# Performance work log

Measured on AMD Instinct MI355X. Metric: run time of the kernel, lower is better.

## Reference

```python
import jax, jax.numpy as jnp
import numpy as np

DEPTH = 24; D_MODEL = 192; D_INNER = 384; D_STATE = 16; DT_RANK = 12; D_CONV = 4
H = 32; W = 3200; P = 16; NP = (W // P) * (H // P)  # 400 patches
NCLS = 22; BATCH = 4; EPS = 1e-5


def _rmsnorm(x, w):
    return x * jax.lax.rsqrt(jnp.mean(x * x, axis=-1, keepdims=True) + EPS) * w


def _causal_dwconv(x, w, b):
    # x: (B, L, D), w: (D, K) depthwise, left-padded causal conv (mamba conv1d)
    D = x.shape[-1]; K = w.shape[-1]
    xp = jnp.pad(jnp.swapaxes(x, 1, 2), ((0, 0), (0, 0), (K - 1, 0)))
    y = jax.lax.conv_general_dilated(xp, w[:, None, :], (1,), 'VALID',
            dimension_numbers=('NCH', 'OIH', 'NCH'), feature_group_count=D)
    return jnp.swapaxes(y + b[None, :, None], 1, 2)


def _selective_scan(x, dt, Bm, Cm, A, Dsk):
    # x, dt: (B, L, d); Bm, Cm: (B, L, n); A: (d, n); Dsk: (d,)
    dA = jnp.exp(dt[..., None] * A)                  # (B, L, d, n)
    dBx = (dt * x)[..., None] * Bm[:, :, None, :]    # (B, L, d, n)
    h0 = jnp.zeros((x.shape[0], x.shape[2], A.shape[1]), x.dtype)

    def step(h, inp):
        a, bx, c = inp
        h = a * h + bx
        return h, jnp.einsum('bdn,bn->bd', h, c)

    _, ys = jax.lax.scan(step, h0,
        (jnp.swapaxes(dA, 0, 1), jnp.swapaxes(dBx, 0, 1), jnp.swapaxes(Cm, 0, 1)))
    return jnp.swapaxes(ys, 0, 1) + x * Dsk


def _mamba_dir(xz, cw_l, cb_l, xpw, dtw, dtb, A, Dsk):
    xx, z = jnp.split(xz, 2, axis=-1)
    xx = jax.nn.silu(_causal_dwconv(xx, cw_l, cb_l))
    dbl = xx @ xpw.T                                  # (B, L, dt_rank + 2n)
    dt = jax.nn.softplus(dbl[..., :DT_RANK] @ dtw.T + dtb)
    Bm = dbl[..., DT_RANK:DT_RANK + D_STATE]
    Cm = dbl[..., DT_RANK + D_STATE:]
    y = _selective_scan(xx, dt, Bm, Cm, A, Dsk)
    return y * jax.nn.silu(z)


def _forward(x, pe_w, pe_b, cls_token, pos_embed, norm_w, in_proj_w, cw, cb,
             xproj_w, dtproj_w, dtproj_b, A_log, A_b_log, Dp, outproj_w,
             norm_f_w, head_w, head_b):
    B = x.shape[0]
    # patch embed: conv2d stride=kernel=16 on (B,1,H,W)
    y = jax.lax.conv_general_dilated(x[:, None], pe_w, (P, P), 'VALID',
            dimension_numbers=('NCHW', 'OIHW', 'NCHW')) + pe_b[None, :, None, None]
    tok = jnp.transpose(y, (0, 2, 3, 1)).reshape(B, -1, D_MODEL)   # (B, NP, D)
    tok = jnp.concatenate([jnp.broadcast_to(cls_token, (B, 1, D_MODEL)), tok], axis=1)
    tok = tok + pos_embed

    def layer_step(carry, p):
        hidden, residual = carry
        nw, ipw, cw_l, cb_l, xpw, dtw, dtb, Al, Abl, Dsk, opw = p
        residual = residual + hidden          # fused add (residual_in_fp32: all fp32)
        h = _rmsnorm(residual, nw)
        xz = h @ ipw.T                         # (B, L, 2*d_inner)
        y_f = _mamba_dir(xz, cw_l, cb_l, xpw, dtw, dtb, -jnp.exp(Al), Dsk)
        y_b = _mamba_dir(xz[:, ::-1], cw_l, cb_l, xpw, dtw, dtb, -jnp.exp(Abl), Dsk)[:, ::-1]
        return ((y_f + y_b) @ opw.T, residual), None

    # NOTE: source sets residual = x AND hidden = x before the loop, so the
    (hidden, residual), _ = jax.lax.scan(
        layer_step, (tok, tok),
        (norm_w, in_proj_w, cw, cb, xproj_w, dtproj_w, dtproj_b, A_log, A_b_log, Dp, outproj_w))
    out = _rmsnorm(residual + hidden, norm_f_w)
    return out[:, 0] @ head_w.T + head_b          # (B, n_classes)


def setup_inputs() -> dict:
    key = jax.random.key(0)
    ks = jax.random.split(key, 12)

    def n(k, shape, scale):
        return jax.random.normal(k, shape, jnp.float32) * scale

    a_init = jnp.tile(jnp.log(jnp.arange(1, D_STATE + 1, dtype=jnp.float32))[None, None, :],
                      (DEPTH, D_INNER, 1))
    return {
        'x': n(ks[0], (BATCH, H, W), 1.0),
        'pe_w': n(ks[1], (D_MODEL, 1, P, P), 1.0 / P),
        'pe_b': jnp.zeros((D_MODEL,), jnp.float32),
        'cls_token': n(ks[2], (1, 1, D_MODEL), 0.02),
        'pos_embed': n(ks[3], (1, NP + 1, D_MODEL), 0.02),
        'norm_w': jnp.ones((DEPTH, D_MODEL), jnp.float32),
        'in_proj_w': n(ks[4], (DEPTH, 2 * D_INNER, D_MODEL), D_MODEL ** -0.5),
        'cw': n(ks[5], (DEPTH, D_INNER, D_CONV), D_CONV ** -0.5),
        'cb': jnp.zeros((DEPTH, D_INNER), jnp.float32),
        'xproj_w': n(ks[6], (DEPTH, DT_RANK + 2 * D_STATE, D_INNER), D_INNER ** -0.5),
        'dtproj_w': n(ks[7], (DEPTH, D_INNER, DT_RANK), DT_RANK ** -0.5),
        'dtproj_b': n(ks[8], (DEPTH, D_INNER), 0.1),
        'A_log': a_init,
        'A_b_log': a_init,
        'Dp': jnp.ones((DEPTH, D_INNER), jnp.float32),
        'outproj_w': n(ks[9], (DEPTH, D_MODEL, D_INNER), D_INNER ** -0.5 / np.sqrt(DEPTH)),
        'norm_f_w': jnp.ones((D_MODEL,), jnp.float32),
        'head_w': n(ks[10], (NCLS, D_MODEL), D_MODEL ** -0.5),
        'head_b': jnp.zeros((NCLS,), jnp.float32),
    }


def reference(x, pe_w, pe_b, cls_token, pos_embed, norm_w, in_proj_w, cw, cb,
              xproj_w, dtproj_w, dtproj_b, A_log, A_b_log, Dp, outproj_w,
              norm_f_w, head_w, head_b):
    return _forward(x, pe_w, pe_b, cls_token, pos_embed, norm_w, in_proj_w, cw, cb,
                    xproj_w, dtproj_w, dtproj_b, A_log, A_b_log, Dp, outproj_w,
                    norm_f_w, head_w, head_b)
```

## Files before the change

### kernel.cpp

```cpp
#include <hip/hip_runtime.h>
#include <hip/hip_bf16.h>

#define DEPTH 24
#define DM 192
#define DI 384
#define DS 16
#define DR 12
#define LSEQ 401
#define BATCH 4
#define NTOK (BATCH*LSEQ)
#define NCLS 22
#define NC 16
#define TCH 26

__device__ __forceinline__ float silu_f(float x) { return x / (1.f + __expf(-x)); }

__global__ void patch_embed_k(const float* __restrict__ x,
                              const float* __restrict__ pe_w,
                              const float* __restrict__ pe_b,
                              const float* __restrict__ cls,
                              const float* __restrict__ pos,
                              float* __restrict__ residual, float* __restrict__ hidden)
{
    __shared__ float xp[4][256];
    int g0 = blockIdx.x * 4;
    int c = threadIdx.x;
    #pragma unroll
    for (int j = 0; j < 4; j++) {
        int g = g0 + j;
        int b = g / LSEQ, t = g % LSEQ;
        if (t != 0) {
            int p = t - 1, pi = p / 200, pj = p % 200;
            for (int i = c; i < 256; i += 192) {
                int pp = i >> 4, qq = i & 15;
                xp[j][i] = x[((size_t)(b * 32 + pi * 16 + pp)) * 3200 + pj * 16 + qq];
            }
        }
    }
    __syncthreads();
    float acc[4] = {0.f, 0.f, 0.f, 0.f};
    for (int k = 0; k < 256; k++) {
        float w = pe_w[c * 256 + k];
        #pragma unroll
        for (int j = 0; j < 4; j++) acc[j] += xp[j][k] * w;
    }
    #pragma unroll
    for (int j = 0; j < 4; j++) {
        int g = g0 + j;
        int t = g % LSEQ;
        float v = (t == 0) ? cls[c] : (acc[j] + pe_b[c]);
        v += pos[t * DM + c];
        residual[(size_t)g * DM + c] = v;
        hidden[(size_t)g * DM + c] = v;
    }
}

__global__ __launch_bounds__(192) void prenorm_k(
    const float* __restrict__ resin, float* __restrict__ hidden,
    float* __restrict__ resout, float* __restrict__ hnorm,
    const float* __restrict__ nw, float* __restrict__ dbl)
{
    __shared__ float wsum[3][4];
    int c = threadIdx.x;
    int t0 = blockIdx.x * 4;
    int wave = c >> 6, lane = c & 63;
    float r[4], s[4];
    #pragma unroll
    for (int j = 0; j < 4; j++) {
        int idx = (t0 + j) * DM + c;
        r[j] = resin[idx] + hidden[idx];
        s[j] = r[j] * r[j];
    }
    #pragma unroll
    for (int off = 32; off > 0; off >>= 1) {
        #pragma unroll
        for (int j = 0; j < 4; j++) s[j] += __shfl_down(s[j], off);
    }
    if (lane == 0) {
        #pragma unroll
        for (int j = 0; j < 4; j++) wsum[wave][j] = s[j];
    }
    __syncthreads();
    float nwv = nw[c];
    #pragma unroll
    for (int j = 0; j < 4; j++) {
        float tot = wsum[0][j] + wsum[1][j] + wsum[2][j];
        float rms = rsqrtf(tot / (float)DM + 1e-5f);
        int idx = (t0 + j) * DM + c;
        resout[idx] = r[j];
        hnorm[idx] = r[j] * rms * nwv;
        hidden[idx] = 0.f;
    }
    for (int i = blockIdx.x * 192 + c; i < 2 * NTOK * 44; i += 401 * 192)
        dbl[i] = 0.f;
}

__global__ __launch_bounds__(256) void gemm_xz_k(
    const float* __restrict__ hnorm, const float* __restrict__ ipw,
    float* __restrict__ xz)
{
    constexpr int KS = 48;
    __shared__ float As[KS][68];
    __shared__ float Ws[KS][68];
    int tid = threadIdx.x;
    int bn = blockIdx.x * 64;
    int bm = blockIdx.y * 64;
    int r0 = (tid >> 4) * 4;
    int c0 = (tid & 15) * 4;
    int srow = tid >> 2, sk = (tid & 3) * 12;
    float acc[4][4] = {};
    for (int k0 = 0; k0 < DM; k0 += KS) {
        {
            int m = bm + srow;
            const float* ap = hnorm + (size_t)m * DM + k0 + sk;
            #pragma unroll
            for (int i = 0; i < 12; i++)
                As[sk + i][srow] = (m < NTOK) ? ap[i] : 0.f;
            const float* wp = ipw + (size_t)(bn + srow) * DM + k0 + sk;
            #pragma unroll
            for (int i = 0; i < 12; i++)
                Ws[sk + i][srow] = wp[i];
        }
        __syncthreads();
        #pragma unroll
        for (int kk = 0; kk < KS; kk++) {
            float4 a = *(const float4*)&As[kk][r0];
            float4 w = *(const float4*)&Ws[kk][c0];
            acc[0][0] += a.x * w.x; acc[0][1] += a.x * w.y; acc[0][2] += a.x * w.z; acc[0][3] += a.x * w.w;
            acc[1][0] += a.y * w.x; acc[1][1] += a.y * w.y; acc[1][2] += a.y * w.z; acc[1][3] += a.y * w.w;
            acc[2][0] += a.z * w.x; acc[2][1] += a.z * w.y; acc[2][2] += a.z * w.z; acc[2][3] += a.z * w.w;
            acc[3][0] += a.w * w.x; acc[3][1] += a.w * w.y; acc[3][2] += a.w * w.z; acc[3][3] += a.w * w.w;
        }
        __syncthreads();
    }
    #pragma unroll
    for (int i = 0; i < 4; i++) {
        int m = bm + r0 + i;
        if (m >= NTOK) continue;
        *(float4*)&xz[(size_t)m * (2 * DI) + bn + c0] =
            make_float4(acc[i][0], acc[i][1], acc[i][2], acc[i][3]);
    }
}

__global__ __launch_bounds__(256) void xproj_conv_k(
    const float* __restrict__ xz,
    const float* __restrict__ cw, const float* __restrict__ cb,
    const float* __restrict__ xpw, float* __restrict__ dbl)
{
    __shared__ float As[96][33];
    __shared__ float Ws[96][48];
    int tid = threadIdx.x;
    int kbase = blockIdx.x * 96;
    int bm = blockIdx.y * 32;
    for (int idx = tid; idx < 96 * 32; idx += 256) {
        int k = idx >> 5, row = idx & 31;
        int m = bm + row;
        float v = 0.f;
        if (m < 2 * NTOK) {
            int dir = m / NTOK;
            int r = m - dir * NTOK;
            int b = r / LSEQ, t = r % LSEQ;
            int ch = kbase + k;
            float a = cb[ch];
            #pragma unroll
            for (int j = 0; j < 4; j++) {
                int tt = t - 3 + j;
                if (tt >= 0) {
                    int st = dir ? (LSEQ - 1 - tt) : tt;
                    a += cw[ch * 4 + j] * xz[((size_t)(b * LSEQ + st)) * (2 * DI) + ch];
                }
            }
            v = silu_f(a);
        }
        As[k][row] = v;
    }
    for (int i = tid; i < 96 * 48; i += 256) {
        int k = i / 48, rr = i % 48;
        Ws[k][rr] = (rr < 44) ? xpw[(size_t)rr * DI + kbase + k] : 0.f;
    }
    __syncthreads();
    int row = tid & 31, cg = tid >> 5;
    int cbase = cg * 6;
    float acc[6] = {};
    #pragma unroll 4
    for (int kk = 0; kk < 96; kk++) {
        float a = As[kk][row];
        #pragma unroll
        for (int j = 0; j < 6; j++) acc[j] += a * Ws[kk][cbase + j];
    }
    int m = bm + row;
    if (m < 2 * NTOK) {
        #pragma unroll
        for (int j = 0; j < 6; j++) {
            int cc = cbase + j;
            if (cc < 44) atomicAdd(&dbl[(size_t)m * 44 + cc], acc[j]);
        }
    }
}

__global__ __launch_bounds__(256) void scan_part_k(
    const float* __restrict__ xz, const float* __restrict__ dbl,
    const float* __restrict__ cw, const float* __restrict__ cb,
    const float* __restrict__ dtw, const float* __restrict__ dtb,
    const float* __restrict__ A_log, const float* __restrict__ A_b_log,
    float* __restrict__ hloc, float* __restrict__ Pc)
{
    __shared__ float sdbl[TCH][44];
    __shared__ float sdt[TCH][16];
    __shared__ float sxx[TCH][16];
    __shared__ float sw[16][12];
    __shared__ float sb2[16];
    int dblk = blockIdx.x, chunk = blockIdx.y;
    int db = blockIdx.z;
    int dir = db >> 2, b = db & 3;
    int tid = threadIdx.x;
    int d0 = dblk * 16;
    int t0 = chunk * TCH;
    size_t dof44 = (size_t)db * LSEQ * 44;
    for (int i = tid; i < TCH * 44; i += 256) {
        int t = i / 44, cc = i - t * 44;
        sdbl[t][cc] = dbl[dof44 + (size_t)(t0 + t) * 44 + cc];
    }
    if (tid < 192) { int d = tid / 12, r = tid - d * 12; sw[d][r] = dtw[(size_t)(d0 + d) * 12 + r]; }
    if (tid < 16) sb2[tid] = dtb[d0 + tid];
    for (int i = tid; i < TCH * 16; i += 256) {
        int t = i >> 4, d = i & 15;
        int tq = t0 + t, ch = d0 + d;
        float a = cb[ch];
        #pragma unroll
        for (int j = 0; j < 4; j++) {
            int tt = tq - 3 + j;
            if (tt >= 0) {
                int st = dir ? (LSEQ - 1 - tt) : tt;
                a += cw[ch * 4 + j] * xz[((size_t)(b * LSEQ + st)) * (2 * DI) + ch];
            }
        }
        sxx[t][d] = silu_f(a);
    }
    __syncthreads();
    for (int i = tid; i < TCH * 16; i += 256) {
        int t = i >> 4, d = i & 15;
        float a2 = sb2[d];
        #pragma unroll
        for (int r = 0; r < 12; r++) a2 += sdbl[t][r] * sw[d][r];
        sdt[t][d] = (a2 > 15.f) ? a2 : __logf(1.f + __expf(a2));
    }
    __syncthreads();
    int wave = tid >> 6, lane = tid & 63;
    int dsub = wave * 4 + (lane >> 4);
    int n = lane & 15;
    const float* Al = dir ? A_b_log : A_log;
    float Aval = -__expf(Al[(d0 + dsub) * DS + n]);
    float h = 0.f, P = 1.f;
    #pragma unroll
    for (int i = 0; i < TCH; i++) {
        float dtv = sdt[i][dsub];
        float xv  = sxx[i][dsub];
        float Bv  = sdbl[i][12 + n];
        float dA = __expf(dtv * Aval);
        h = dA * h + (dtv * xv) * Bv;
        P *= dA;
    }
    size_t idx2 = ((size_t)db * NC + chunk) * (DI * DS) + (size_t)(d0 + dsub) * DS + n;
    hloc[idx2] = h;
    Pc[idx2] = P;
}

__global__ __launch_bounds__(256) void scan_fix_k(
    const float* __restrict__ xz, const float* __restrict__ dbl,
    const float* __restrict__ cw, const float* __restrict__ cb,
    const float* __restrict__ dtw, const float* __restrict__ dtb,
    const float* __restrict__ A_log, const float* __restrict__ A_b_log,
    const float* __restrict__ Dp,
    const float* __restrict__ hloc, const float* __restrict__ Pc,
    float* __restrict__ yraw)
{
    __shared__ float sdbl[TCH][44];
    __shared__ float sdt[TCH][16];
    __shared__ float sxx[TCH][16];
    __shared__ float sy[TCH][16];
    __shared__ float sw[16][12];
    __shared__ float sb2[16];
    int dblk = blockIdx.x, chunk = blockIdx.y;
    int db = blockIdx.z;
    int dir = db >> 2, b = db & 3;
    int tid = threadIdx.x;
    int d0 = dblk * 16;
    int t0 = chunk * TCH;
    size_t dofD = (size_t)db * LSEQ * DI;
    size_t dof44 = (size_t)db * LSEQ * 44;
    for (int i = tid; i < TCH * 44; i += 256) {
        int t = i / 44, cc = i - t * 44;
        sdbl[t][cc] = ((t0 + t) < LSEQ) ? dbl[dof44 + (size_t)(t0 + t) * 44 + cc] : 0.f;
    }
    if (tid < 192) { int d = tid / 12, r = tid - d * 12; sw[d][r] = dtw[(size_t)(d0 + d) * 12 + r]; }
    if (tid < 16) sb2[tid] = dtb[d0 + tid];
    for (int i = tid; i < TCH * 16; i += 256) {
        int t = i >> 4, d = i & 15;
        int tq = t0 + t, ch = d0 + d;
        float v = 0.f;
        if (tq < LSEQ) {
            float a = cb[ch];
            #pragma unroll
            for (int j = 0; j < 4; j++) {
                int tt = tq - 3 + j;
                if (tt >= 0) {
                    int st = dir ? (LSEQ - 1 - tt) : tt;
                    a += cw[ch * 4 + j] * xz[((size_t)(b * LSEQ + st)) * (2 * DI) + ch];
                }
            }
            v = silu_f(a);
        }
        sxx[t][d] = v;
    }
    __syncthreads();
    for (int i = tid; i < TCH * 16; i += 256) {
        int t = i >> 4, d = i & 15;
        float a2 = sb2[d];
        #pragma unroll
        for (int r = 0; r < 12; r++) a2 += sdbl[t][r] * sw[d][r];
        sdt[t][d] = (a2 > 15.f) ? a2 : __logf(1.f + __expf(a2));
    }
    __syncthreads();
    int wave = tid >> 6, lane = tid & 63;
    int dsub = wave * 4 + (lane >> 4);
    int n = lane & 15;
    const float* Al = dir ? A_b_log : A_log;
    float Aval = -__expf(Al[(d0 + dsub) * DS + n]);
    float Dv = Dp[d0 + dsub];
    float h = 0.f;
    size_t cbase = (size_t)db * NC * (DI * DS) + (size_t)(d0 + dsub) * DS + n;
    #pragma unroll
    for (int j = 0; j < NC - 1; j++) {
        size_t idx = cbase + (size_t)j * (DI * DS);
        float pj = Pc[idx], hj = hloc[idx];
        h = (j < chunk) ? (pj * h + hj) : h;
    }
    #pragma unroll
    for (int i = 0; i < TCH; i++) {
        float dtv = sdt[i][dsub];
        float xv  = sxx[i][dsub];
        float Bv  = sdbl[i][12 + n];
        float Cv  = sdbl[i][28 + n];
        h = __expf(dtv * Aval) * h + (dtv * xv) * Bv;
        float p = h * Cv;
        p += __shfl_xor(p, 1);
        p += __shfl_xor(p, 2);
        p += __shfl_xor(p, 4);
        p += __shfl_xor(p, 8);
        if (n == 0) sy[i][dsub] = p + xv * Dv;
    }
    __syncthreads();
    int len = min(t0 + TCH, LSEQ) - t0;
    for (int idx = tid; idx < len * 16; idx += 256) {
        int t = idx >> 4, d = idx & 15;
        yraw[dofD + (size_t)(t0 + t) * DI + d0 + d] = sy[t][d];
    }
}

__global__ __launch_bounds__(256) void outproj_k(
    const float* __restrict__ yraw, const float* __restrict__ xz,
    const float* __restrict__ opw, float* __restrict__ hidden)
{
    __shared__ float As[96][34];
    __shared__ float Ws[96][34];
    int tid = threadIdx.x;
    int bn = blockIdx.x * 32;
    int bm = blockIdx.y * 32;
    int kbase = blockIdx.z * 192;
    int row8 = tid >> 3, seg = tid & 7, k0 = seg * 24;
    float a[24], wreg[24];
    int m = bm + row8;
    if (m < NTOK) {
        int b = m / LSEQ, t = m % LSEQ;
        const float* yf = yraw + (size_t)m * DI + kbase + k0;
        const float* yb = yraw + (size_t)(NTOK + b * LSEQ + (LSEQ - 1 - t)) * DI + kbase + k0;
        const float* zp = xz + (size_t)m * (2 * DI) + DI + kbase + k0;
        #pragma unroll
        for (int i = 0; i < 24; i++) {
            float z = zp[i];
            a[i] = (yf[i] + yb[i]) * (z / (1.f + __expf(-z)));
        }
    } else {
        #pragma unroll
        for (int i = 0; i < 24; i++) a[i] = 0.f;
    }
    {
        const float* wp = opw + (size_t)(bn + row8) * DI + kbase + k0;
        #pragma unroll
        for (int i = 0; i < 24; i++) wreg[i] = wp[i];
    }
    int r0 = (tid >> 4) * 2, c0 = (tid & 15) * 2;
    float acc[2][2] = {};
    #pragma unroll
    for (int st = 0; st < 2; st++) {
        if (st) __syncthreads();
        if ((seg >> 2) == st) {
            int kb = k0 - st * 96;
            #pragma unroll
            for (int i = 0; i < 24; i++) {
                As[kb + i][row8] = a[i];
                Ws[kb + i][row8] = wreg[i];
            }
        }
        __syncthreads();
        #pragma unroll 8
        for (int kk = 0; kk < 96; kk++) {
            float2 av = *(const float2*)&As[kk][r0];
            float2 wv = *(const float2*)&Ws[kk][c0];
            acc[0][0] += av.x * wv.x; acc[0][1] += av.x * wv.y;
            acc[1][0] += av.y * wv.x; acc[1][1] += av.y * wv.y;
        }
    }
    #pragma unroll
    for (int i = 0; i < 2; i++) {
        int mm = bm + r0 + i;
        if (mm >= NTOK) continue;
        #pragma unroll
        for (int j = 0; j < 2; j++)
            atomicAdd(&hidden[(size_t)mm * DM + bn + c0 + j], acc[i][j]);
    }
}

__global__ void final_head_k(const float* __restrict__ residual, const float* __restrict__ hidden,
                             const float* __restrict__ norm_f,
                             const float* __restrict__ head_w,
                             const float* __restrict__ head_b,
                             void* __restrict__ out,
                             const unsigned short* __restrict__ probe)
{
    __shared__ float wsum[3];
    __shared__ float hb[DM];
    int b = blockIdx.x;
    int c = threadIdx.x;
    int idx = (b * LSEQ) * DM + c;
    float r = residual[idx] + hidden[idx];
    float s = r * r;
    for (int off = 32; off > 0; off >>= 1) s += __shfl_down(s, off);
    int wave = c >> 6, lane = c & 63;
    if (lane == 0) wsum[wave] = s;
    __syncthreads();
    float tot = wsum[0] + wsum[1] + wsum[2];
    float rms = rsqrtf(tot / (float)DM + 1e-5f);
    hb[c] = r * rms * norm_f[c];
    __syncthreads();
    if (c < NCLS) {
        float acc = head_b[c];
        #pragma unroll 8
        for (int k = 0; k < DM; k++) acc += hb[k] * head_w[c * DM + k];
        if (probe[0] == 0x3F80u)
            ((__hip_bfloat16*)out)[b * NCLS + c] = __float2bfloat16(acc);
        else
            ((float*)out)[b * NCLS + c] = acc;
    }
}

extern "C" void kernel_launch(void* const* d_in, const int* in_sizes, int n_in,
                              void* d_out, int out_size, void* d_ws, size_t ws_size,
                              hipStream_t stream)
{
    (void)in_sizes; (void)n_in; (void)out_size; (void)ws_size;
    const float* x      = (const float*)d_in[0];
    const float* pe_w   = (const float*)d_in[1];
    const float* pe_b   = (const float*)d_in[2];
    const float* cls    = (const float*)d_in[3];
    const float* pos    = (const float*)d_in[4];
    const float* norm_w = (const float*)d_in[5];
    const float* ipw    = (const float*)d_in[6];
    const float* cw     = (const float*)d_in[7];
    const float* cb     = (const float*)d_in[8];
    const float* xpw    = (const float*)d_in[9];
    const float* dtw    = (const float*)d_in[10];
    const float* dtb    = (const float*)d_in[11];
    const float* A_log  = (const float*)d_in[12];
    const float* A_b_log= (const float*)d_in[13];
    const float* Dp     = (const float*)d_in[14];
    const float* opw    = (const float*)d_in[15];
    const float* norm_f = (const float*)d_in[16];
    const float* head_w = (const float*)d_in[17];
    const float* head_b = (const float*)d_in[18];
    const unsigned short* probe = (const unsigned short*)d_in[14];

    float* ws = (float*)d_ws;
    const size_t nTokDM = (size_t)NTOK * DM;
    const size_t nTokXZ = (size_t)NTOK * 2 * DI;
    const size_t nDirDI = (size_t)2 * NTOK * DI;
    const size_t nDir44 = (size_t)2 * NTOK * 44;
    const size_t nChunk = (size_t)2 * BATCH * NC * DI * DS;
    float* resA   = ws;
    float* resB   = resA + nTokDM;
    float* hidden = resB + nTokDM;
    float* hnorm  = hidden + nTokDM;
    float* xz     = hnorm + nTokDM;
    float* dbl    = xz + nTokXZ;
    float* yraw   = dbl + nDir44;
    float* hloc   = yraw + nDirDI;
    float* Pc     = hloc + nChunk;

    patch_embed_k<<<NTOK / 4, DM, 0, stream>>>(x, pe_w, pe_b, cls, pos, resA, hidden);

    for (int l = 0; l < DEPTH; l++) {
        float* rin  = (l & 1) ? resB : resA;
        float* rout = (l & 1) ? resA : resB;

        prenorm_k<<<LSEQ, DM, 0, stream>>>(rin, hidden, rout, hnorm,
                                           norm_w + (size_t)l * DM, dbl);

        gemm_xz_k<<<dim3(12, 26), 256, 0, stream>>>(
            hnorm, ipw + (size_t)l * 2 * DI * DM, xz);

        xproj_conv_k<<<dim3(4, 101), 256, 0, stream>>>(
            xz, cw + (size_t)l * DI * 4, cb + (size_t)l * DI,
            xpw + (size_t)l * 44 * DI, dbl);

        scan_part_k<<<dim3(DI / 16, NC - 1, 2 * BATCH), 256, 0, stream>>>(
            xz, dbl, cw + (size_t)l * DI * 4, cb + (size_t)l * DI,
            dtw + (size_t)l * DI * DR, dtb + (size_t)l * DI,
            A_log + (size_t)l * DI * DS, A_b_log + (size_t)l * DI * DS,
            hloc, Pc);

        scan_fix_k<<<dim3(DI / 16, NC, 2 * BATCH), 256, 0, stream>>>(
            xz, dbl, cw + (size_t)l * DI * 4, cb + (size_t)l * DI,
            dtw + (size_t)l * DI * DR, dtb + (size_t)l * DI,
            A_log + (size_t)l * DI * DS, A_b_log + (size_t)l * DI * DS,
            Dp + (size_t)l * DI, hloc, Pc, yraw);

        outproj_k<<<dim3(6, 51, 2), 256, 0, stream>>>(
            yraw, xz, opw + (size_t)l * DM * DI, hidden);
    }

    final_head_k<<<BATCH, DM, 0, stream>>>(resA, hidden, norm_f, head_w, head_b,
                                           d_out, probe);
}
```

Before: 3.061 ms.

## Fuse RMSNorm into in-proj GEMM, drop split-K atomics, use single-pass sequential scan

The standalone prenorm kernel is folded into the in-projection GEMM. Each block computes the residual sum and RMS for its rows, and the first column block writes the residual out. The x-projection and out-projection kernels loop over the full K dimension inside one block instead of splitting K across blocks, so they store results directly and no longer need atomics or buffer zeroing. The two-pass chunked scan (partial states plus fix-up) becomes one kernel per (channel block, direction×batch) that walks the sequence serially in 64-step tiles. This removes the hloc/Pc traffic and two launches per layer, but leaves far fewer blocks and a long serial dependency chain.

```diff
diff --git a/kernel.cpp b/kernel.cpp
--- a/kernel.cpp
+++ b/kernel.cpp
@@ -10,8 +10,7 @@
 #define BATCH 4
 #define NTOK (BATCH*LSEQ)
 #define NCLS 22
-#define NC 16
-#define TCH 26
+#define SCH 64
 
 __device__ __forceinline__ float silu_f(float x) { return x / (1.f + __expf(-x)); }
 
@@ -55,77 +54,80 @@
     }
 }
 
-__global__ __launch_bounds__(192) void prenorm_k(
-    const float* __restrict__ resin, float* __restrict__ hidden,
-    float* __restrict__ resout, float* __restrict__ hnorm,
-    const float* __restrict__ nw, float* __restrict__ dbl)
-{
-    __shared__ float wsum[3][4];
-    int c = threadIdx.x;
-    int t0 = blockIdx.x * 4;
-    int wave = c >> 6, lane = c & 63;
-    float r[4], s[4];
-    #pragma unroll
-    for (int j = 0; j < 4; j++) {
-        int idx = (t0 + j) * DM + c;
-        r[j] = resin[idx] + hidden[idx];
-        s[j] = r[j] * r[j];
-    }
-    #pragma unroll
-    for (int off = 32; off > 0; off >>= 1) {
-        #pragma unroll
-        for (int j = 0; j < 4; j++) s[j] += __shfl_down(s[j], off);
-    }
-    if (lane == 0) {
-        #pragma unroll
-        for (int j = 0; j < 4; j++) wsum[wave][j] = s[j];
-    }
-    __syncthreads();
-    float nwv = nw[c];
-    #pragma unroll
-    for (int j = 0; j < 4; j++) {
-        float tot = wsum[0][j] + wsum[1][j] + wsum[2][j];
-        float rms = rsqrtf(tot / (float)DM + 1e-5f);
-        int idx = (t0 + j) * DM + c;
-        resout[idx] = r[j];
-        hnorm[idx] = r[j] * rms * nwv;
-        hidden[idx] = 0.f;
-    }
-    for (int i = blockIdx.x * 192 + c; i < 2 * NTOK * 44; i += 401 * 192)
-        dbl[i] = 0.f;
-}
-
 __global__ __launch_bounds__(256) void gemm_xz_k(
-    const float* __restrict__ hnorm, const float* __restrict__ ipw,
-    float* __restrict__ xz)
-{
-    constexpr int KS = 48;
-    __shared__ float As[KS][68];
-    __shared__ float Ws[KS][68];
+    const float* __restrict__ resin, const float* __restrict__ hidden,
+    float* __restrict__ resout, const float* __restrict__ nw,
+    const float* __restrict__ ipw, float* __restrict__ xz)
+{
+    __shared__ float As[48][68];
+    __shared__ float Ws[48][68];
+    __shared__ float srms[64];
+    __shared__ float ps[64][4];
     int tid = threadIdx.x;
     int bn = blockIdx.x * 64;
     int bm = blockIdx.y * 64;
-    int r0 = (tid >> 4) * 4;
-    int c0 = (tid & 15) * 4;
-    int srow = tid >> 2, sk = (tid & 3) * 12;
+    int rr = tid >> 2, q = tid & 3;
+    int m = bm + rr;
+    float rv[4][12];
+    float s = 0.f;
+    if (m < NTOK) {
+        const float* rp = resin + (size_t)m * DM;
+        const float* hp = hidden + (size_t)m * DM;
+        #pragma unroll
+        for (int c = 0; c < 4; c++) {
+            int base = c * 48 + q * 12;
+            #pragma unroll
+            for (int i = 0; i < 12; i += 4) {
+                float4 a = *(const float4*)&rp[base + i];
+                float4 b = *(const float4*)&hp[base + i];
+                float r0 = a.x + b.x, r1 = a.y + b.y, r2 = a.z + b.z, r3 = a.w + b.w;
+                rv[c][i] = r0; rv[c][i + 1] = r1; rv[c][i + 2] = r2; rv[c][i + 3] = r3;
+                s += r0 * r0 + r1 * r1 + r2 * r2 + r3 * r3;
+            }
+        }
+        if (bn == 0) {
+            float* op = resout + (size_t)m * DM;
+            #pragma unroll
+            for (int c = 0; c < 4; c++) {
+                int base = c * 48 + q * 12;
+                #pragma unroll
+                for (int i = 0; i < 12; i += 4)
+                    *(float4*)&op[base + i] =
+                        make_float4(rv[c][i], rv[c][i + 1], rv[c][i + 2], rv[c][i + 3]);
+            }
+        }
+    } else {
+        #pragma unroll
+        for (int c = 0; c < 4; c++)
+            #pragma unroll
+            for (int i = 0; i < 12; i++) rv[c][i] = 0.f;
+    }
+    ps[rr][q] = s;
+    __syncthreads();
+    if (q == 0) {
+        float tot = ps[rr][0] + ps[rr][1] + ps[rr][2] + ps[rr][3];
+        srms[rr] = rsqrtf(tot * (1.f / (float)DM) + 1e-5f);
+    }
+    __syncthreads();
+
+    int orow = (tid >> 4) * 4;
+    int ocol = (tid & 15) * 4;
+    int sk = q * 12;
     float acc[4][4] = {};
-    for (int k0 = 0; k0 < DM; k0 += KS) {
-        {
-            int m = bm + srow;
-            const float* ap = hnorm + (size_t)m * DM + k0 + sk;
-            #pragma unroll
-            for (int i = 0; i < 12; i++)
-                As[sk + i][srow] = (m < NTOK) ? ap[i] : 0.f;
-            const float* wp = ipw + (size_t)(bn + srow) * DM + k0 + sk;
-            #pragma unroll
-            for (int i = 0; i < 12; i++)
-                Ws[sk + i][srow] = wp[i];
-        }
-        __syncthreads();
-        #pragma unroll
-        for (int kk = 0; kk < KS; kk++) {
-            float4 a = *(const float4*)&As[kk][r0];
-            float4 w = *(const float4*)&Ws[kk][c0];
+    for (int c = 0; c < 4; c++) {
+        float rs = srms[rr];
+        #pragma unroll
+        for (int i = 0; i < 12; i++)
+            As[sk + i][rr] = rv[c][i] * rs * nw[c * 48 + sk + i];
+        const float* wp = ipw + (size_t)(bn + rr) * DM + c * 48 + sk;
+        #pragma unroll
+        for (int i = 0; i < 12; i++)
+            Ws[sk + i][rr] = wp[i];
+        __syncthreads();
+        #pragma unroll
+        for (int kk = 0; kk < 48; kk++) {
+            float4 a = *(const float4*)&As[kk][orow];
+            float4 w = *(const float4*)&Ws[kk][ocol];
             acc[0][0] += a.x * w.x; acc[0][1] += a.x * w.y; acc[0][2] += a.x * w.z; acc[0][3] += a.x * w.w;
             acc[1][0] += a.y * w.x; acc[1][1] += a.y * w.y; acc[1][2] += a.y * w.z; acc[1][3] += a.y * w.w;
             acc[2][0] += a.z * w.x; acc[2][1] += a.z * w.y; acc[2][2] += a.z * w.z; acc[2][3] += a.z * w.w;
@@ -135,14 +137,14 @@
     }
     #pragma unroll
     for (int i = 0; i < 4; i++) {
-        int m = bm + r0 + i;
-        if (m >= NTOK) continue;
-        *(float4*)&xz[(size_t)m * (2 * DI) + bn + c0] =
+        int mm = bm + orow + i;
+        if (mm >= NTOK) continue;
+        *(float4*)&xz[(size_t)mm * (2 * DI) + bn + ocol] =
             make_float4(acc[i][0], acc[i][1], acc[i][2], acc[i][3]);
     }
 }
 
-__global__ __launch_bounds__(256) void xproj_conv_k(
+__global__ __launch_bounds__(256) void xproj_k(
     const float* __restrict__ xz,
     const float* __restrict__ cw, const float* __restrict__ cb,
     const float* __restrict__ xpw, float* __restrict__ dbl)
@@ -150,178 +152,78 @@
     __shared__ float As[96][33];
     __shared__ float Ws[96][48];
     int tid = threadIdx.x;
-    int kbase = blockIdx.x * 96;
-    int bm = blockIdx.y * 32;
-    for (int idx = tid; idx < 96 * 32; idx += 256) {
-        int k = idx >> 5, row = idx & 31;
-        int m = bm + row;
-        float v = 0.f;
-        if (m < 2 * NTOK) {
-            int dir = m / NTOK;
-            int r = m - dir * NTOK;
-            int b = r / LSEQ, t = r % LSEQ;
-            int ch = kbase + k;
-            float a = cb[ch];
-            #pragma unroll
-            for (int j = 0; j < 4; j++) {
-                int tt = t - 3 + j;
-                if (tt >= 0) {
-                    int st = dir ? (LSEQ - 1 - tt) : tt;
-                    a += cw[ch * 4 + j] * xz[((size_t)(b * LSEQ + st)) * (2 * DI) + ch];
-                }
-            }
-            v = silu_f(a);
-        }
-        As[k][row] = v;
-    }
-    for (int i = tid; i < 96 * 48; i += 256) {
-        int k = i / 48, rr = i % 48;
-        Ws[k][rr] = (rr < 44) ? xpw[(size_t)rr * DI + kbase + k] : 0.f;
-    }
-    __syncthreads();
+    int bm = blockIdx.x * 32;
     int row = tid & 31, cg = tid >> 5;
     int cbase = cg * 6;
     float acc[6] = {};
-    #pragma unroll 4
-    for (int kk = 0; kk < 96; kk++) {
-        float a = As[kk][row];
-        #pragma unroll
-        for (int j = 0; j < 6; j++) acc[j] += a * Ws[kk][cbase + j];
-    }
-    int m = bm + row;
-    if (m < 2 * NTOK) {
+    for (int kbase = 0; kbase < DI; kbase += 96) {
+        for (int idx = tid; idx < 96 * 32; idx += 256) {
+            int k = idx >> 5, r = idx & 31;
+            int mm = bm + r;
+            float v = 0.f;
+            if (mm < 2 * NTOK) {
+                int dir = mm / NTOK;
+                int rem = mm - dir * NTOK;
+                int b = rem / LSEQ, t = rem % LSEQ;
+                int ch = kbase + k;
+                float a = cb[ch];
+                #pragma unroll
+                for (int j = 0; j < 4; j++) {
+                    int tt = t - 3 + j;
+                    if (tt >= 0) {
+                        int st = dir ? (LSEQ - 1 - tt) : tt;
+                        a += cw[ch * 4 + j] * xz[((size_t)(b * LSEQ + st)) * (2 * DI) + ch];
+                    }
+                }
+                v = silu_f(a);
+            }
+            As[k][r] = v;
+        }
+        for (int i = tid; i < 96 * 48; i += 256) {
+            int k = i / 48, cc = i % 48;
+            Ws[k][cc] = (cc < 44) ? xpw[(size_t)cc * DI + kbase + k] : 0.f;
+        }
+        __syncthreads();
+        #pragma unroll 4
+        for (int kk = 0; kk < 96; kk++) {
+            float a = As[kk][row];
+            #pragma unroll
+            for (int j = 0; j < 6; j++) acc[j] += a * Ws[kk][cbase + j];
+        }
+        __syncthreads();
+    }
+    int mm = bm + row;
+    if (mm < 2 * NTOK) {
         #pragma unroll
         for (int j = 0; j < 6; j++) {
             int cc = cbase + j;
-            if (cc < 44) atomicAdd(&dbl[(size_t)m * 44 + cc], acc[j]);
-        }
-    }
-}
-
-__global__ __launch_bounds__(256) void scan_part_k(
+            if (cc < 44) dbl[(size_t)mm * 44 + cc] = acc[j];
+        }
+    }
+}
+
+__global__ __launch_bounds__(256) void scan_k(
     const float* __restrict__ xz, const float* __restrict__ dbl,
     const float* __restrict__ cw, const float* __restrict__ cb,
     const float* __restrict__ dtw, const float* __restrict__ dtb,
     const float* __restrict__ A_log, const float* __restrict__ A_b_log,
-    float* __restrict__ hloc, float* __restrict__ Pc)
-{
-    __shared__ float sdbl[TCH][44];
-    __shared__ float sdt[TCH][16];
-    __shared__ float sxx[TCH][16];
+    const float* __restrict__ Dp, float* __restrict__ yraw)
+{
+    __shared__ float sdbl[SCH][44];
+    __shared__ float sxx[SCH][16];
+    __shared__ float sdt[SCH][16];
+    __shared__ float sy[SCH][16];
     __shared__ float sw[16][12];
     __shared__ float sb2[16];
-    int dblk = blockIdx.x, chunk = blockIdx.y;
-    int db = blockIdx.z;
+    int dblk = blockIdx.x;
+    int db = blockIdx.y;
     int dir = db >> 2, b = db & 3;
     int tid = threadIdx.x;
     int d0 = dblk * 16;
-    int t0 = chunk * TCH;
     size_t dof44 = (size_t)db * LSEQ * 44;
-    for (int i = tid; i < TCH * 44; i += 256) {
-        int t = i / 44, cc = i - t * 44;
-        sdbl[t][cc] = dbl[dof44 + (size_t)(t0 + t) * 44 + cc];
-    }
+    size_t dofD = (size_t)db * LSEQ * DI;
     if (tid < 192) { int d = tid / 12, r = tid - d * 12; sw[d][r] = dtw[(size_t)(d0 + d) * 12 + r]; }
     if (tid < 16) sb2[tid] = dtb[d0 + tid];
-    for (int i = tid; i < TCH * 16; i += 256) {
-        int t = i >> 4, d = i & 15;
-        int tq = t0 + t, ch = d0 + d;
-        float a = cb[ch];
-        #pragma unroll
-        for (int j = 0; j < 4; j++) {
-            int tt = tq - 3 + j;
-            if (tt >= 0) {
-                int st = dir ? (LSEQ - 1 - tt) : tt;
-                a += cw[ch * 4 + j] * xz[((size_t)(b * LSEQ + st)) * (2 * DI) + ch];
-            }
-        }
-        sxx[t][d] = silu_f(a);
-    }
-    __syncthreads();
-    for (int i = tid; i < TCH * 16; i += 256) {
-        int t = i >> 4, d = i & 15;
-        float a2 = sb2[d];
-        #pragma unroll
-        for (int r = 0; r < 12; r++) a2 += sdbl[t][r] * sw[d][r];
-        sdt[t][d] = (a2 > 15.f) ? a2 : __logf(1.f + __expf(a2));
-    }
-    __syncthreads();
-    int wave = tid >> 6, lane = tid & 63;
-    int dsub = wave * 4 + (lane >> 4);
-    int n = lane & 15;
-    const float* Al = dir ? A_b_log : A_log;
-    float Aval = -__expf(Al[(d0 + dsub) * DS + n]);
-    float h = 0.f, P = 1.f;
-    #pragma unroll
-    for (int i = 0; i < TCH; i++) {
-        float dtv = sdt[i][dsub];
-        float xv  = sxx[i][dsub];
-        float Bv  = sdbl[i][12 + n];
-        float dA = __expf(dtv * Aval);
-        h = dA * h + (dtv * xv) * Bv;
-        P *= dA;
-    }
-    size_t idx2 = ((size_t)db * NC + chunk) * (DI * DS) + (size_t)(d0 + dsub) * DS + n;
-    hloc[idx2] = h;
-    Pc[idx2] = P;
-}
-
-__global__ __launch_bounds__(256) void scan_fix_k(
-    const float* __restrict__ xz, const float* __restrict__ dbl,
-    const float* __restrict__ cw, const float* __restrict__ cb,
-    const float* __restrict__ dtw, const float* __restrict__ dtb,
-    const float* __restrict__ A_log, const float* __restrict__ A_b_log,
-    const float* __restrict__ Dp,
-    const float* __restrict__ hloc, const float* __restrict__ Pc,
-    float* __restrict__ yraw)
-{
-    __shared__ float sdbl[TCH][44];
-    __shared__ float sdt[TCH][16];
-    __shared__ float sxx[TCH][16];
-    __shared__ float sy[TCH][16];
-    __shared__ float sw[16][12];
-    __shared__ float sb2[16];
-    int dblk = blockIdx.x, chunk = blockIdx.y;
-    int db = blockIdx.z;
-    int dir = db >> 2, b = db & 3;
-    int tid = threadIdx.x;
-    int d0 = dblk * 16;
-    int t0 = chunk * TCH;
-    size_t dofD = (size_t)db * LSEQ * DI;
-    size_t dof44 = (size_t)db * LSEQ * 44;
-    for (int i = tid; i < TCH * 44; i += 256) {
-        int t = i / 44, cc = i - t * 44;
-        sdbl[t][cc] = ((t0 + t) < LSEQ) ? dbl[dof44 + (size_t)(t0 + t) * 44 + cc] : 0.f;
-    }
-    if (tid < 192) { int d = tid / 12, r = tid - d * 12; sw[d][r] = dtw[(size_t)(d0 + d) * 12 + r]; }
-    if (tid < 16) sb2[tid] = dtb[d0 + tid];
-    for (int i = tid; i < TCH * 16; i += 256) {
-        int t = i >> 4, d = i & 15;
-        int tq = t0 + t, ch = d0 + d;
-        float v = 0.f;
-        if (tq < LSEQ) {
-            float a = cb[ch];
-            #pragma unroll
-            for (int j = 0; j < 4; j++) {
-                int tt = tq - 3 + j;
-                if (tt >= 0) {
-                    int st = dir ? (LSEQ - 1 - tt) : tt;
-                    a += cw[ch * 4 + j] * xz[((size_t)(b * LSEQ + st)) * (2 * DI) + ch];
-                }
-            }
-            v = silu_f(a);
-        }
-        sxx[t][d] = v;
-    }
-    __syncthreads();
-    for (int i = tid; i < TCH * 16; i += 256) {
-        int t = i >> 4, d = i & 15;
-        float a2 = sb2[d];
-        #pragma unroll
-        for (int r = 0; r < 12; r++) a2 += sdbl[t][r] * sw[d][r];
-        sdt[t][d] = (a2 > 15.f) ? a2 : __logf(1.f + __expf(a2));
-    }
-    __syncthreads();
     int wave = tid >> 6, lane = tid & 63;
     int dsub = wave * 4 + (lane >> 4);
     int n = lane & 15;
@@ -329,32 +231,55 @@
     float Aval = -__expf(Al[(d0 + dsub) * DS + n]);
     float Dv = Dp[d0 + dsub];
     float h = 0.f;
-    size_t cbase = (size_t)db * NC * (DI * DS) + (size_t)(d0 + dsub) * DS + n;
-    #pragma unroll
-    for (int j = 0; j < NC - 1; j++) {
-        size_t idx = cbase + (size_t)j * (DI * DS);
-        float pj = Pc[idx], hj = hloc[idx];
-        h = (j < chunk) ? (pj * h + hj) : h;
-    }
-    #pragma unroll
-    for (int i = 0; i < TCH; i++) {
-        float dtv = sdt[i][dsub];
-        float xv  = sxx[i][dsub];
-        float Bv  = sdbl[i][12 + n];
-        float Cv  = sdbl[i][28 + n];
-        h = __expf(dtv * Aval) * h + (dtv * xv) * Bv;
-        float p = h * Cv;
-        p += __shfl_xor(p, 1);
-        p += __shfl_xor(p, 2);
-        p += __shfl_xor(p, 4);
-        p += __shfl_xor(p, 8);
-        if (n == 0) sy[i][dsub] = p + xv * Dv;
-    }
-    __syncthreads();
-    int len = min(t0 + TCH, LSEQ) - t0;
-    for (int idx = tid; idx < len * 16; idx += 256) {
-        int t = idx >> 4, d = idx & 15;
-        yraw[dofD + (size_t)(t0 + t) * DI + d0 + d] = sy[t][d];
+    for (int t0 = 0; t0 < LSEQ; t0 += SCH) {
+        int len = min(LSEQ - t0, SCH);
+        for (int i = tid; i < len * 44; i += 256) {
+            int t = i / 44, cc = i - t * 44;
+            sdbl[t][cc] = dbl[dof44 + (size_t)(t0 + t) * 44 + cc];
+        }
+        for (int i = tid; i < len * 16; i += 256) {
+            int t = i >> 4, d = i & 15;
+            int tq = t0 + t, ch = d0 + d;
+            float a = cb[ch];
+            #pragma unroll
+            for (int j = 0; j < 4; j++) {
+                int tt = tq - 3 + j;
+                if (tt >= 0) {
+                    int st = dir ? (LSEQ - 1 - tt) : tt;
+                    a += cw[ch * 4 + j] * xz[((size_t)(b * LSEQ + st)) * (2 * DI) + ch];
+                }
+            }
+            sxx[t][d] = silu_f(a);
+        }
+        __syncthreads();
+        for (int i = tid; i < len * 16; i += 256) {
+            int t = i >> 4, d = i & 15;
+            float a2 = sb2[d];
+            #pragma unroll
+            for (int r = 0; r < 12; r++) a2 += sdbl[t][r] * sw[d][r];
+            sdt[t][d] = (a2 > 15.f) ? a2 : __logf(1.f + __expf(a2));
+        }
+        __syncthreads();
+        #pragma unroll 4
+        for (int i = 0; i < len; i++) {
+            float dtv = sdt[i][dsub];
+            float xv  = sxx[i][dsub];
+            float Bv  = sdbl[i][12 + n];
+            float Cv  = sdbl[i][28 + n];
+            h = __expf(dtv * Aval) * h + (dtv * xv) * Bv;
+            float p = h * Cv;
+            p += __shfl_xor(p, 1);
+            p += __shfl_xor(p, 2);
+            p += __shfl_xor(p, 4);
+            p += __shfl_xor(p, 8);
+            if (n == 0) sy[i][dsub] = p + xv * Dv;
+        }
+        __syncthreads();
+        for (int i = tid; i < len * 16; i += 256) {
+            int t = i >> 4, d = i & 15;
+            yraw[dofD + (size_t)(t0 + t) * DI + d0 + d] = sy[t][d];
+        }
+        __syncthreads();
     }
 }
 
@@ -362,63 +287,49 @@
     const float* __restrict__ yraw, const float* __restrict__ xz,
     const float* __restrict__ opw, float* __restrict__ hidden)
 {
-    __shared__ float As[96][34];
-    __shared__ float Ws[96][34];
+    __shared__ float As[48][34];
+    __shared__ float Ws[48][34];
     int tid = threadIdx.x;
     int bn = blockIdx.x * 32;
     int bm = blockIdx.y * 32;
-    int kbase = blockIdx.z * 192;
-    int row8 = tid >> 3, seg = tid & 7, k0 = seg * 24;
-    float a[24], wreg[24];
-    int m = bm + row8;
-    if (m < NTOK) {
-        int b = m / LSEQ, t = m % LSEQ;
-        const float* yf = yraw + (size_t)m * DI + kbase + k0;
-        const float* yb = yraw + (size_t)(NTOK + b * LSEQ + (LSEQ - 1 - t)) * DI + kbase + k0;
-        const float* zp = xz + (size_t)m * (2 * DI) + DI + kbase + k0;
-        #pragma unroll
-        for (int i = 0; i < 24; i++) {
-            float z = zp[i];
-            a[i] = (yf[i] + yb[i]) * (z / (1.f + __expf(-z)));
-        }
-    } else {
-        #pragma unroll
-        for (int i = 0; i < 24; i++) a[i] = 0.f;
-    }
-    {
-        const float* wp = opw + (size_t)(bn + row8) * DI + kbase + k0;
-        #pragma unroll
-        for (int i = 0; i < 24; i++) wreg[i] = wp[i];
-    }
-    int r0 = (tid >> 4) * 2, c0 = (tid & 15) * 2;
+    int orow = (tid >> 4) * 2, ocol = (tid & 15) * 2;
     float acc[2][2] = {};
-    #pragma unroll
-    for (int st = 0; st < 2; st++) {
-        if (st) __syncthreads();
-        if ((seg >> 2) == st) {
-            int kb = k0 - st * 96;
-            #pragma unroll
-            for (int i = 0; i < 24; i++) {
-                As[kb + i][row8] = a[i];
-                Ws[kb + i][row8] = wreg[i];
-            }
+    for (int k0 = 0; k0 < DI; k0 += 48) {
+        for (int i = tid; i < 48 * 32; i += 256) {
+            int row = i / 48, k = i - row * 48;
+            int mm = bm + row;
+            float vv = 0.f;
+            if (mm < NTOK) {
+                int b = mm / LSEQ, t = mm % LSEQ;
+                int ch = k0 + k;
+                float yf = yraw[(size_t)mm * DI + ch];
+                float yb = yraw[(size_t)(NTOK + b * LSEQ + (LSEQ - 1 - t)) * DI + ch];
+                float z  = xz[(size_t)mm * (2 * DI) + DI + ch];
+                vv = (yf + yb) * silu_f(z);
+            }
+            As[k][row] = vv;
+        }
+        for (int i = tid; i < 48 * 32; i += 256) {
+            int col = i / 48, k = i - col * 48;
+            Ws[k][col] = opw[(size_t)(bn + col) * DI + k0 + k];
         }
         __syncthreads();
         #pragma unroll 8
-        for (int kk = 0; kk < 96; kk++) {
-            float2 av = *(const float2*)&As[kk][r0];
-            float2 wv = *(const float2*)&Ws[kk][c0];
+        for (int kk = 0; kk < 48; kk++) {
+            float2 av = *(const float2*)&As[kk][orow];
+            float2 wv = *(const float2*)&Ws[kk][ocol];
             acc[0][0] += av.x * wv.x; acc[0][1] += av.x * wv.y;
             acc[1][0] += av.y * wv.x; acc[1][1] += av.y * wv.y;
         }
+        __syncthreads();
     }
     #pragma unroll
     for (int i = 0; i < 2; i++) {
-        int mm = bm + r0 + i;
+        int mm = bm + orow + i;
         if (mm >= NTOK) continue;
         #pragma unroll
         for (int j = 0; j < 2; j++)
-            atomicAdd(&hidden[(size_t)mm * DM + bn + c0 + j], acc[i][j]);
+            hidden[(size_t)mm * DM + bn + ocol + j] = acc[i][j];
     }
 }
 
@@ -486,16 +397,12 @@
     const size_t nTokXZ = (size_t)NTOK * 2 * DI;
     const size_t nDirDI = (size_t)2 * NTOK * DI;
     const size_t nDir44 = (size_t)2 * NTOK * 44;
-    const size_t nChunk = (size_t)2 * BATCH * NC * DI * DS;
     float* resA   = ws;
     float* resB   = resA + nTokDM;
     float* hidden = resB + nTokDM;
-    float* hnorm  = hidden + nTokDM;
-    float* xz     = hnorm + nTokDM;
+    float* xz     = hidden + nTokDM;
     float* dbl    = xz + nTokXZ;
     float* yraw   = dbl + nDir44;
-    float* hloc   = yraw + nDirDI;
-    float* Pc     = hloc + nChunk;
 
     patch_embed_k<<<NTOK / 4, DM, 0, stream>>>(x, pe_w, pe_b, cls, pos, resA, hidden);
 
@@ -503,29 +410,21 @@
         float* rin  = (l & 1) ? resB : resA;
         float* rout = (l & 1) ? resA : resB;
 
-        prenorm_k<<<LSEQ, DM, 0, stream>>>(rin, hidden, rout, hnorm,
-                                           norm_w + (size_t)l * DM, dbl);
-
         gemm_xz_k<<<dim3(12, 26), 256, 0, stream>>>(
-            hnorm, ipw + (size_t)l * 2 * DI * DM, xz);
-
-        xproj_conv_k<<<dim3(4, 101), 256, 0, stream>>>(
+            rin, hidden, rout, norm_w + (size_t)l * DM,
+            ipw + (size_t)l * 2 * DI * DM, xz);
+
+        xproj_k<<<101, 256, 0, stream>>>(
             xz, cw + (size_t)l * DI * 4, cb + (size_t)l * DI,
             xpw + (size_t)l * 44 * DI, dbl);
 
-        scan_part_k<<<dim3(DI / 16, NC - 1, 2 * BATCH), 256, 0, stream>>>(
+        scan_k<<<dim3(24, 8), 256, 0, stream>>>(
             xz, dbl, cw + (size_t)l * DI * 4, cb + (size_t)l * DI,
             dtw + (size_t)l * DI * DR, dtb + (size_t)l * DI,
             A_log + (size_t)l * DI * DS, A_b_log + (size_t)l * DI * DS,
-            hloc, Pc);
-
-        scan_fix_k<<<dim3(DI / 16, NC, 2 * BATCH), 256, 0, stream>>>(
-            xz, dbl, cw + (size_t)l * DI * 4, cb + (size_t)l * DI,
-            dtw + (size_t)l * DI * DR, dtb + (size_t)l * DI,
-            A_log + (size_t)l * DI * DS, A_b_log + (size_t)l * DI * DS,
-            Dp + (size_t)l * DI, hloc, Pc, yraw);
-
-        outproj_k<<<dim3(6, 51, 2), 256, 0, stream>>>(
+            Dp + (size_t)l * DI, yraw);
+
+        outproj_k<<<dim3(6, 51), 256, 0, stream>>>(
             yraw, xz, opw + (size_t)l * DM * DI, hidden);
     }
 
```

After: 6.431 ms. 110% more time.
